# Kernel tuning notes

Measured on AMD Instinct MI355X. Metric: run time of the kernel, lower is better.

## Reference

```python
import jax, jax.numpy as jnp
import numpy as np

ANCHOR_SIZES = (128.0, 256.0, 512.0)
ANCHOR_RATIOS = (0.5, 1.0, 2.0)
IOU_THR = 0.3


def _conv(x, w, b, pad):
    y = jax.lax.conv_general_dilated(
        x, w, window_strides=(1, 1), padding=[(pad, pad), (pad, pad)],
        dimension_numbers=("NCHW", "OIHW", "NCHW"))
    return y + b[None, :, None, None]


def _make_anchors(grid_h, grid_w, stride):
    # torchvision-style cell anchors (ratio-major over scales), rounded
    scales = jnp.asarray(ANCHOR_SIZES, jnp.float32)
    ratios = jnp.asarray(ANCHOR_RATIOS, jnp.float32)
    h_r = jnp.sqrt(ratios)
    w_r = 1.0 / h_r
    ws = (w_r[:, None] * scales[None, :]).reshape(-1)  # (A,)
    hs = (h_r[:, None] * scales[None, :]).reshape(-1)
    base = jnp.round(jnp.stack([-ws, -hs, ws, hs], axis=1) / 2.0)  # (A,4)
    sx = jnp.arange(grid_w, dtype=jnp.float32) * stride
    sy = jnp.arange(grid_h, dtype=jnp.float32) * stride
    yy, xx = jnp.meshgrid(sy, sx, indexing="ij")
    shifts = jnp.stack([xx, yy, xx, yy], axis=-1).reshape(-1, 4)  # (HW,4)
    return (shifts[:, None, :] + base[None, :, :]).reshape(-1, 4)  # (HW*A,4)


def _apply_box(anchors, deltas):
    w = anchors[:, 2] - anchors[:, 0]
    h = anchors[:, 3] - anchors[:, 1]
    cx = anchors[:, 0] + 0.5 * w
    cy = anchors[:, 1] + 0.5 * h
    pcx = deltas[:, 0] * w + cx
    pcy = deltas[:, 1] * h + cy
    pw = jnp.exp(deltas[:, 2]) * w
    ph = jnp.exp(deltas[:, 3]) * h
    return jnp.stack([pcx - 0.5 * pw, pcy - 0.5 * ph,
                      pcx + 0.5 * pw, pcy + 0.5 * ph], axis=1)


def _clip(boxes, img_h, img_w):
    x1 = jnp.clip(boxes[:, 0], 0.0, img_w)
    y1 = jnp.clip(boxes[:, 1], 0.0, img_h)
    x2 = jnp.clip(boxes[:, 2], 0.0, img_w)
    y2 = jnp.clip(boxes[:, 3], 0.0, img_h)
    return jnp.stack([x1, y1, x2, y2], axis=1)


def _nms_keep(boxes, scores, thr):
    # returns boolean keep mask in ORIGINAL box order (all idxs identical in
    # the source's batched_nms call, so this is plain NMS)
    n = boxes.shape[0]
    order = jnp.argsort(-scores)
    b = boxes[order]
    area = (b[:, 2] - b[:, 0]) * (b[:, 3] - b[:, 1])
    lt = jnp.maximum(b[:, None, :2], b[None, :, :2])
    rb = jnp.minimum(b[:, None, 2:], b[None, :, 2:])
    wh = jnp.clip(rb - lt, 0.0, None)
    inter = wh[..., 0] * wh[..., 1]
    iou = inter / (area[:, None] + area[None, :] - inter + 1e-9)  # (N,N)
    idx = jnp.arange(n)

    def body(i, keep):
        sup = (iou[i] > thr) & (idx > i)
        return jnp.where(keep[i], keep & ~sup, keep)

    keep_sorted = jax.lax.fori_loop(0, n, body, jnp.ones(n, bool))
    return jnp.zeros(n, bool).at[order].set(keep_sorted)


def setup_inputs() -> dict:
    key = jax.random.key(0)
    ks = jax.random.split(key, 7)
    C, H, W = 256, 32, 32
    A = len(ANCHOR_SIZES) * len(ANCHOR_RATIOS)  # 9
    return {
        "features": jax.random.normal(ks[0], (1, C, H, W), jnp.float32),
        "image_size": 512,
        "conv_w": jax.random.normal(ks[1], (512, C, 3, 3), jnp.float32) * 0.01,
        "conv_b": jnp.zeros((512,), jnp.float32),
        "cls_w": jax.random.normal(ks[2], (2 * A, 512, 1, 1), jnp.float32) * 0.01,
        "cls_b": jnp.zeros((2 * A,), jnp.float32),
        "bbox_w": jax.random.normal(ks[3], (4 * A, 512, 1, 1), jnp.float32) * 0.01,
        "bbox_b": jnp.zeros((4 * A,), jnp.float32),
    }


def reference(features, image_size, conv_w, conv_b, cls_w, cls_b, bbox_w, bbox_b):
    img_h = img_w = float(image_size)
    x = jax.nn.relu(_conv(features, conv_w, conv_b, pad=1))
    logits = _conv(x, cls_w, cls_b, pad=0)          # (1, 2A, H, W)
    bbox_pred = _conv(x, bbox_w, bbox_b, pad=0)     # (1, 4A, H, W)
    probs = jax.nn.sigmoid(logits)
    fg_scores = probs[:, 1::2, :, :].reshape(-1)    # same flatten order as torch
    grid_h, grid_w = features.shape[2], features.shape[3]
    stride = image_size // grid_h
    anchors = _make_anchors(grid_h, grid_w, float(stride))
    proposals = _apply_box(anchors, bbox_pred.reshape(-1, 4))
    proposals = _clip(proposals, img_h, img_w)
    keep = _nms_keep(proposals, fg_scores, IOU_THR)
    # fixed-shape output: suppressed boxes zeroed, plus the keep mask
    return proposals * keep[:, None].astype(proposals.dtype), probs, keep
```

## Files before the change

kernel.cpp:

```cpp
#include <hip/hip_runtime.h>
#include <math.h>

#define X_B      0
#define BBOX_B   2097152
#define PROPS_B  2244608
#define KEYS_B   2392064
#define RANK_B   2465792
#define SKEYS_B  2502656
#define SBOX_B   2576384
#define MASK_B   2725888
#define WS_NEED  13400000

typedef unsigned long long u64;
typedef double v4d __attribute__((ext_vector_type(4)));

__global__ __launch_bounds__(256, 2) void conv3x3_mfma_k(
    const float* __restrict__ feat, const float* __restrict__ w,
    const float* __restrict__ bias, float* __restrict__ xout)
{
  __shared__ float wl[9280];
  __shared__ float fl[8768];

  const int tid = threadIdx.x;
  const int bid = blockIdx.x;
  const int ct = ((bid & 7) << 2) | ((bid >> 3) >> 4);
  const int g  = (bid >> 3) & 15;
  const int co0 = ct << 4;
  const int y0  = g << 1;

  for (int i = tid; i < 8768; i += 256) fl[i] = 0.0f;

  const int lane = tid & 63, wv = tid >> 6;
  const int q = lane >> 4, n = lane & 15;
  const int wy = wv >> 1, xb = (wv & 1) << 4;
  const int xn = xb + n;

  v4d ac0 = {0.0, 0.0, 0.0, 0.0}, ac1 = {0.0, 0.0, 0.0, 0.0};
  v4d ac2 = {0.0, 0.0, 0.0, 0.0}, ac3 = {0.0, 0.0, 0.0, 0.0};
  const float4* feat4 = (const float4*)feat;

  __syncthreads();

  for (int c = 0; c < 4; ++c) {
    const int cb = c << 6;
    #pragma unroll
    for (int i = 0; i < 9; ++i) {
      const int idx4 = tid + (i << 8);
      const int co = idx4 / 144;
      const int s4 = idx4 - co * 144;
      *(float4*)&wl[co * 580 + (s4 << 2)] =
          *(const float4*)(w + (co0 + co) * 2304 + c * 576 + (s4 << 2));
    }
    #pragma unroll
    for (int i = 0; i < 8; ++i) {
      const int idx4 = tid + (i << 8);
      const int ci = idx4 >> 5;
      const int rr = (idx4 >> 3) & 3;
      const int x4 = idx4 & 7;
      const int grow = y0 - 1 + rr;
      if ((unsigned)grow < 32u) {
        const float4 v = feat4[((cb + ci) << 8) + (grow << 3) + x4];
        float* p = &fl[ci * 137 + rr * 34 + 1 + (x4 << 2)];
        p[0] = v.x; p[1] = v.y; p[2] = v.z; p[3] = v.w;
      }
    }
    __syncthreads();
    #pragma unroll
    for (int tap = 0; tap < 9; ++tap) {
      const int ky = tap / 3, kx = tap - 3 * (tap / 3);
      const float* ab = &wl[n * 580 + q * 9 + tap];
      const float* bb = &fl[q * 137 + (wy + ky) * 34 + xn + kx];
      #pragma unroll
      for (int u = 0; u < 16; u += 4) {
        ac0 = __builtin_amdgcn_mfma_f64_16x16x4f64(
            (double)ab[(u + 0) * 36], (double)bb[(u + 0) * 548], ac0, 0, 0, 0);
        ac1 = __builtin_amdgcn_mfma_f64_16x16x4f64(
            (double)ab[(u + 1) * 36], (double)bb[(u + 1) * 548], ac1, 0, 0, 0);
        ac2 = __builtin_amdgcn_mfma_f64_16x16x4f64(
            (double)ab[(u + 2) * 36], (double)bb[(u + 2) * 548], ac2, 0, 0, 0);
        ac3 = __builtin_amdgcn_mfma_f64_16x16x4f64(
            (double)ab[(u + 3) * 36], (double)bb[(u + 3) * 548], ac3, 0, 0, 0);
      }
    }
    __syncthreads();
  }

  const int pbase = (g << 6) + (wv << 4) + n;
  #pragma unroll
  for (int i = 0; i < 4; ++i) {
    const int co = co0 + q + (i << 2);
    const double s = (ac0[i] + ac1[i]) + (ac2[i] + ac3[i]);
    const double v = fmax(s + (double)bias[co], 0.0);
    xout[(co << 10) + pbase] = (float)v;
  }
}

#define CPITCH 38
#define CCHS   (18 * CPITCH)
__global__ __launch_bounds__(256) void conv3x3_relu_fb_k(
    const float* __restrict__ feat, const float* __restrict__ w,
    const float* __restrict__ bias, float* __restrict__ xout)
{
  __shared__ float il[2][8 * CCHS];
  const int cp = blockIdx.x >> 1, h = blockIdx.x & 1;
  const int tid = threadIdx.x;
  const int h16 = h << 4;
  const int co0 = cp << 1;
  for (int i = tid; i < 8 * CCHS; i += 256) { il[0][i] = 0.0f; il[1][i] = 0.0f; }
  const int yl = tid >> 4;
  const int x0 = (tid & 15) << 1;
  double aA0 = 0.0, aA1 = 0.0, aB0 = 0.0, aB1 = 0.0;
  const float4* feat4 = (const float4*)feat;
  float4 pf[5]; int pch[5], pt[5], pc4[5], pok[5];
  #pragma unroll
  for (int k = 0; k < 5; ++k) {
    const int i = tid + (k << 8);
    const int ch = i / 144, rem = i - ch * 144;
    const int t = rem >> 3, c4 = rem & 7;
    const int g = h16 - 1 + t;
    pch[k] = ch; pt[k] = t; pc4[k] = c4;
    pok[k] = (i < 1152) && ((unsigned)g < 32u);
    pf[k] = pok[k] ? feat4[(ch << 8) + (g << 3) + c4] : float4{0.f,0.f,0.f,0.f};
  }
  __syncthreads();
  for (int cc = 0; cc < 256; cc += 8) {
    const int buf = (cc >> 3) & 1;
    #pragma unroll
    for (int k = 0; k < 5; ++k)
      if (pok[k]) {
        float* p = &il[buf][pch[k] * CCHS + pt[k] * CPITCH + (pc4[k] << 2) + 1];
        p[0] = pf[k].x; p[1] = pf[k].y; p[2] = pf[k].z; p[3] = pf[k].w;
      }
    if (cc + 8 < 256) {
      #pragma unroll
      for (int k = 0; k < 5; ++k) {
        const int g = h16 - 1 + pt[k];
        if (pok[k]) pf[k] = feat4[((cc + 8 + pch[k]) << 8) + (g << 3) + pc4[k]];
      }
    }
    __syncthreads();
    #pragma unroll
    for (int cl = 0; cl < 8; ++cl) {
      const float* wAp = w + co0 * 2304 + (cc + cl) * 9;
      const float* wBp = wAp + 2304;
      double wa[9], wb[9];
      #pragma unroll
      for (int q = 0; q < 9; ++q) { wa[q] = (double)wAp[q]; wb[q] = (double)wBp[q]; }
      const float* ir = &il[buf][cl * CCHS + yl * CPITCH + x0];
      #pragma unroll
      for (int ky = 0; ky < 3; ++ky) {
        const float2 q0 = *(const float2*)(ir + ky * CPITCH);
        const float2 q1 = *(const float2*)(ir + ky * CPITCH + 2);
        const double v0 = (double)q0.x, v1 = (double)q0.y;
        const double v2 = (double)q1.x, v3 = (double)q1.y;
        aA0 += v0 * wa[3*ky+0] + v1 * wa[3*ky+1] + v2 * wa[3*ky+2];
        aA1 += v1 * wa[3*ky+0] + v2 * wa[3*ky+1] + v3 * wa[3*ky+2];
        aB0 += v0 * wb[3*ky+0] + v1 * wb[3*ky+1] + v2 * wb[3*ky+2];
        aB1 += v1 * wb[3*ky+0] + v2 * wb[3*ky+1] + v3 * wb[3*ky+2];
      }
    }
  }
  const double bA = (double)bias[co0], bB = (double)bias[co0 + 1];
  const int y = h16 + yl;
  float2 rA, rB;
  rA.x = (float)fmax(aA0 + bA, 0.0); rA.y = (float)fmax(aA1 + bA, 0.0);
  rB.x = (float)fmax(aB0 + bB, 0.0); rB.y = (float)fmax(aB1 + bB, 0.0);
  *(float2*)&xout[(co0 << 10) + (y << 5) + x0] = rA;
  *(float2*)&xout[((co0 + 1) << 10) + (y << 5) + x0] = rB;
}

__global__ __launch_bounds__(256) void head1x1_k(
    const float* __restrict__ x,
    const float* __restrict__ cls_w, const float* __restrict__ cls_b,
    const float* __restrict__ bbox_w, const float* __restrict__ bbox_b,
    float* __restrict__ out, float* __restrict__ bbox_out)
{
  __shared__ float wl[512];
  const int bid = blockIdx.x;
  const int co = bid >> 2;
  const int px = ((bid & 3) << 8) | threadIdx.x;
  const bool is_cls = co < 18;
  const float* wsrc = is_cls ? (cls_w + co * 512) : (bbox_w + (co - 18) * 512);
  for (int i = threadIdx.x; i < 512; i += 256) wl[i] = wsrc[i];
  __syncthreads();
  double acc0 = 0.0, acc1 = 0.0, acc2 = 0.0, acc3 = 0.0;
  #pragma unroll 4
  for (int c = 0; c < 512; c += 4) {
    acc0 += (double)x[((c + 0) << 10) | px] * (double)wl[c + 0];
    acc1 += (double)x[((c + 1) << 10) | px] * (double)wl[c + 1];
    acc2 += (double)x[((c + 2) << 10) | px] * (double)wl[c + 2];
    acc3 += (double)x[((c + 3) << 10) | px] * (double)wl[c + 3];
  }
  double acc = ((acc0 + acc1) + (acc2 + acc3)) +
               (double)(is_cls ? cls_b[co] : bbox_b[co - 18]);
  if (is_cls)
    out[36864 + (co << 10) + px] = (float)(1.0 / (1.0 + exp(-acc)));
  else
    bbox_out[((co - 18) << 10) + px] = (float)acc;
}

__global__ __launch_bounds__(256) void proposals_k(
    const float* __restrict__ bbox, const int* __restrict__ imgsz,
    const float* __restrict__ out, float* __restrict__ props,
    u64* __restrict__ keys, unsigned* __restrict__ rank)
{
  const int r = blockIdx.x * 256 + threadIdx.x;
  if (r >= 9216) return;
  const float4 d = ((const float4*)bbox)[r];
  const int cell = r / 9, a = r - cell * 9;
  const int ix = cell & 31, iy = cell >> 5;
  const int ri = a / 3, si = a - ri * 3;
  const double ratio = (ri == 0) ? 0.5 : (ri == 1 ? 1.0 : 2.0);
  const double scale = (si == 0) ? 128.0 : (si == 1 ? 256.0 : 512.0);
  const double hr = sqrt(ratio), wr = 1.0 / hr;
  const double bx = nearbyint(wr * scale * 0.5);
  const double by = nearbyint(hr * scale * 0.5);
  const double cx = ix * 16.0, cy = iy * 16.0;
  const double w = 2.0 * bx, hh = 2.0 * by;
  const double pcx = (double)d.x * w + cx;
  const double pcy = (double)d.y * hh + cy;
  const double pw = exp((double)d.z) * w;
  const double ph = exp((double)d.w) * hh;
  const double im = (double)imgsz[0];
  float4 o;
  o.x = (float)fmin(fmax(pcx - 0.5 * pw, 0.0), im);
  o.y = (float)fmin(fmax(pcy - 0.5 * ph, 0.0), im);
  o.z = (float)fmin(fmax(pcx + 0.5 * pw, 0.0), im);
  o.w = (float)fmin(fmax(pcy + 0.5 * ph, 0.0), im);
  ((float4*)props)[r] = o;
  const float s = out[36864 + ((2 * (r >> 10) + 1) << 10) + (r & 1023)];
  keys[r] = ((u64)__float_as_uint(s) << 32) | (unsigned)(0x7FFFFFFF - r);
  rank[r] = 0u;
}

__global__ __launch_bounds__(256) void rank_k(
    const u64* __restrict__ keys, unsigned* __restrict__ rank)
{
  const int jt = blockIdx.x % 36, ic = blockIdx.x / 36;
  const int j = jt * 256 + threadIdx.x;
  const u64 kj = keys[j];
  const int lane = threadIdx.x & 63;
  const int base = ic * 576;
  unsigned lo[9], hi[9];
  #pragma unroll
  for (int rr = 0; rr < 9; ++rr) {
    const u64 k = keys[base + rr * 64 + lane];
    lo[rr] = (unsigned)k; hi[rr] = (unsigned)(k >> 32);
  }
  unsigned cnt = 0;
  #pragma unroll
  for (int rr = 0; rr < 9; ++rr) {
    #pragma unroll
    for (int l = 0; l < 64; ++l) {
      const unsigned llo = (unsigned)__builtin_amdgcn_readlane((int)lo[rr], l);
      const unsigned lhi = (unsigned)__builtin_amdgcn_readlane((int)hi[rr], l);
      const u64 ki = ((u64)lhi << 32) | llo;
      cnt += (ki > kj) ? 1u : 0u;
    }
  }
  atomicAdd(&rank[j], cnt);
}

__global__ __launch_bounds__(256) void scatter_k(
    const u64* __restrict__ keys, const unsigned* __restrict__ rank,
    const float* __restrict__ props, u64* __restrict__ skeys,
    float4* __restrict__ sboxes)
{
  const int r = blockIdx.x * 256 + threadIdx.x;
  if (r >= 9216) return;
  const unsigned rk = rank[r];
  skeys[rk] = keys[r];
  sboxes[rk] = ((const float4*)props)[r];
}

__global__ __launch_bounds__(256) void mask_k(
    const float4* __restrict__ sb4, u64* __restrict__ mask)
{
  __shared__ __align__(16) float4 ib[64];
  const int ci = blockIdx.x;
  const int Wb = blockIdx.y << 2;
  const int i_lo = ci << 6;
  const int i_hi = min(i_lo + 64, (Wb + 4) << 6);
  if (i_lo >= i_hi) return;
  const int wv = threadIdx.x >> 6, lane = threadIdx.x & 63;
  const int W = Wb + wv;
  const int cnt = i_hi - i_lo;
  if (threadIdx.x < cnt) ib[threadIdx.x] = sb4[i_lo + threadIdx.x];
  __syncthreads();
  const float4 bj = sb4[(W << 6) + lane];
  const float areaJ = (bj.z - bj.x) * (bj.w - bj.y);
  const int n = i_hi - i_lo;
  #pragma unroll 8
  for (int k = 0; k < n; ++k) {
    const float4 bi = ib[k];
    const float areaI = (bi.z - bi.x) * (bi.w - bi.y);
    const float ix1 = fmaxf(bj.x, bi.x), iy1 = fmaxf(bj.y, bi.y);
    const float ix2 = fminf(bj.z, bi.z), iy2 = fminf(bj.w, bi.w);
    const float iw = fmaxf(ix2 - ix1, 0.0f), ih = fmaxf(iy2 - iy1, 0.0f);
    const double inter = (double)iw * (double)ih;
    const double uni = (double)areaJ + (double)areaI - inter + 1e-9;
    const bool pred = inter > 0.3 * uni;
    const u64 bal = __ballot(pred);
    const int i = i_lo + k;
    if (lane == 0) mask[(size_t)i * 144 + W] = bal;
  }
}

__global__ __launch_bounds__(1024) void sweep_out_k(
    const u64* __restrict__ mask, const u64* __restrict__ skeys,
    const float4* __restrict__ sboxes, float* __restrict__ out)
{
  extern __shared__ __align__(16) char sm[];
  u64* subm   = (u64*)sm;
  u64* supAll = subm + 9216;
  u64* keptS  = supAll + 144;
  unsigned short* kpl = (unsigned short*)(keptS + 144);
  int* kcnt  = (int*)(kpl + 9216);
  int* kprev = kcnt + 1;

  const int tid = threadIdx.x;
  const int lane = tid & 63, wv = tid >> 6;
  if (tid == 0) { *kcnt = 0; *kprev = 0; }
  if (tid < 144) { keptS[tid] = 0ULL; supAll[tid] = 0ULL; }
  if (tid < 512) {
    const int wq = tid & 7, r0 = tid >> 3;
    #pragma unroll
    for (int k = 0; k < 8; ++k) {
      const int i = r0 + (k << 6);
      subm[i * 9 + wq] = mask[(size_t)i * 144 + wq];
    }
  }
  __syncthreads();

  for (int sg = 0; sg < 18; ++sg) {
    const int buf = sg & 1;
    const int wbase = sg << 3;
    const int ibase = wbase << 6;
    const int P = *kprev, K = *kcnt;
    if (K > P) {
      const int nW = 144 - wbase;
      const int S = 1024 / nW;
      const int wi = tid % nW, sl = tid / nW;
      if (sl < S) {
        u64 acc = 0ULL;
        for (int j = P + sl; j < K; j += S)
          acc |= mask[(size_t)kpl[j] * 144 + wbase + wi];
        if (acc) atomicOr(&supAll[wbase + wi], acc);
      }
    }
    __syncthreads();
    if (wv == 0) {
      u64 myAlive = (lane < 8) ? ~supAll[wbase + lane] : 0ULL;
      const u64* sub = subm + buf * 4608;
      for (int w = 0; w < 8; ++w) {
        const u64 av = __shfl(myAlive, w, 64);
        if (av == 0ULL) continue;
        const u64 rowL = sub[((w << 6) + lane) * 9 + w];
        u64 cand = av, keptw = 0ULL;
        while (cand) {
          const int b = (int)__builtin_ctzll(cand);
          keptw |= 1ULL << b;
          const u64 sup =
              ((u64)(unsigned)__builtin_amdgcn_readlane((int)(rowL >> 32), b)
               << 32) |
              (unsigned)__builtin_amdgcn_readlane((int)rowL, b);
          cand &= ~(sup | (1ULL << b));
        }
        if (lane == 0) keptS[wbase + w] = keptw;
        if (keptw) {
          const int K2 = *kcnt;
          if ((keptw >> lane) & 1ULL) {
            const int pre =
                __builtin_popcountll(keptw & ((1ULL << lane) - 1ULL));
            kpl[K2 + pre] = (unsigned short)(ibase + (w << 6) + lane);
          }
          if (lane == 0) *kcnt = K2 + __builtin_popcountll(keptw);
          u64 t = keptw;
          while (t) {
            int bs[8]; int nn = 0;
            #pragma unroll
            for (int s = 0; s < 8; ++s) {
              if (t) { bs[s] = (int)__builtin_ctzll(t); t &= t - 1ULL; nn = s + 1; }
              else bs[s] = 0;
            }
            const int kk = lane >> 3, wq = lane & 7;
            u64 r = (kk < nn) ? sub[((w << 6) + bs[kk]) * 9 + wq] : 0ULL;
            r |= __shfl_down(r, 8, 64);
            r |= __shfl_down(r, 16, 64);
            r |= __shfl_down(r, 32, 64);
            myAlive &= ~r;
          }
        }
      }
    } else if (wv == 1) {
      if (lane == 0) *kprev = K;
    } else if (wv >= 8 && sg + 1 < 18) {
      const int s = tid - 512;
      const int wq = s & 7, r0 = s >> 3;
      const int nb = 1 - buf;
      const int ib2 = (sg + 1) << 9;
      const int wb2 = (sg + 1) << 3;
      #pragma unroll
      for (int k = 0; k < 8; ++k) {
        const int i = r0 + (k << 6);
        subm[nb * 4608 + i * 9 + wq] = mask[(size_t)(ib2 + i) * 144 + wb2 + wq];
      }
    }
    __syncthreads();
  }
  for (int i = tid; i < 9216; i += 1024) {
    const u64 key = skeys[i];
    const int orig = 0x7FFFFFFF - (int)(unsigned)(key & 0xFFFFFFFFULL);
    const bool kp = (keptS[i >> 6] >> (i & 63)) & 1ULL;
    float4 ob = sboxes[i];
    if (!kp) { ob.x = 0.f; ob.y = 0.f; ob.z = 0.f; ob.w = 0.f; }
    ((float4*)out)[orig] = ob;
    out[55296 + orig] = kp ? 1.0f : 0.0f;
  }
}

__global__ __launch_bounds__(1024) void nms_fallback_k(
    const float* __restrict__ props, float* __restrict__ out)
{
  __shared__ u64 wmax[16];
  __shared__ float4 curBoxS;
  const int tid = threadIdx.x, wid = tid >> 6, lane = tid & 63;
  u64 key[9];
  float4 box[9];
  #pragma unroll
  for (int j = 0; j < 9; ++j) {
    const int r = tid + (j << 10);
    box[j] = ((const float4*)props)[r];
    const float s = out[36864 + ((2 * (r >> 10) + 1) << 10) + (r & 1023)];
    key[j] = ((u64)__float_as_uint(s) << 32) | (unsigned)(0x7FFFFFFF - r);
  }
  unsigned kept = 0;
  for (;;) {
    u64 m = key[0];
    #pragma unroll
    for (int j = 1; j < 9; ++j) m = key[j] > m ? key[j] : m;
    #pragma unroll
    for (int off = 32; off; off >>= 1) {
      const u64 o = __shfl_down(m, off, 64);
      if (o > m) m = o;
    }
    if (lane == 0) wmax[wid] = m;
    __syncthreads();
    u64 K = wmax[0];
    #pragma unroll
    for (int wv2 = 1; wv2 < 16; ++wv2) { const u64 t = wmax[wv2]; if (t > K) K = t; }
    if (K == 0) break;
    #pragma unroll
    for (int j = 0; j < 9; ++j)
      if (key[j] == K) { curBoxS = box[j]; key[j] = 0; kept |= 1u << j; }
    __syncthreads();
    const float4 cb = curBoxS;
    const float areaC = (cb.z - cb.x) * (cb.w - cb.y);
    #pragma unroll
    for (int j = 0; j < 9; ++j) {
      if (key[j]) {
        const float4 b = box[j];
        const float ix1 = fmaxf(b.x, cb.x), iy1 = fmaxf(b.y, cb.y);
        const float ix2 = fminf(b.z, cb.z), iy2 = fminf(b.w, cb.w);
        const float iw = fmaxf(ix2 - ix1, 0.0f), ih = fmaxf(iy2 - iy1, 0.0f);
        const float areaB = (b.z - b.x) * (b.w - b.y);
        const double inter = (double)iw * (double)ih;
        const double uni = (double)areaB + (double)areaC - inter + 1e-9;
        if (inter > 0.3 * uni) key[j] = 0;
      }
    }
    __syncthreads();
  }
  #pragma unroll
  for (int j = 0; j < 9; ++j) {
    const int r = tid + (j << 10);
    const bool kp = (kept >> j) & 1u;
    float4 ob = box[j];
    if (!kp) { ob.x = 0.f; ob.y = 0.f; ob.z = 0.f; ob.w = 0.f; }
    ((float4*)out)[r] = ob;
    out[55296 + r] = kp ? 1.0f : 0.0f;
  }
}

extern "C" void kernel_launch(void* const* d_in, const int* in_sizes, int n_in,
                              void* d_out, int out_size, void* d_ws, size_t ws_size,
                              hipStream_t stream)
{
  const float* feat   = (const float*)d_in[0];
  const int*   imgsz  = (const int*)d_in[1];
  const float* conv_w = (const float*)d_in[2];
  const float* conv_b = (const float*)d_in[3];
  const float* cls_w  = (const float*)d_in[4];
  const float* cls_b  = (const float*)d_in[5];
  const float* bbox_w = (const float*)d_in[6];
  const float* bbox_b = (const float*)d_in[7];
  float* out = (float*)d_out;
  char*  ws  = (char*)d_ws;
  float* x      = (float*)(ws + X_B);
  float* bbox   = (float*)(ws + BBOX_B);
  float* props  = (float*)(ws + PROPS_B);
  u64*      keys  = (u64*)(ws + KEYS_B);
  unsigned* rankp = (unsigned*)(ws + RANK_B);
  u64*      skeys = (u64*)(ws + SKEYS_B);
  float4*   sboxs = (float4*)(ws + SBOX_B);
  u64*      maskp = (u64*)(ws + MASK_B);

  if (ws_size >= (size_t)WS_NEED) {
    hipLaunchKernelGGL(conv3x3_mfma_k, dim3(512), dim3(256), 0, stream,
                       feat, conv_w, conv_b, x);
    hipLaunchKernelGGL(head1x1_k, dim3(216), dim3(256), 0, stream,
                       x, cls_w, cls_b, bbox_w, bbox_b, out, bbox);
    hipLaunchKernelGGL(proposals_k, dim3(36), dim3(256), 0, stream,
                       bbox, imgsz, out, props, keys, rankp);
    hipLaunchKernelGGL(rank_k, dim3(576), dim3(256), 0, stream, keys, rankp);
    hipLaunchKernelGGL(scatter_k, dim3(36), dim3(256), 0, stream,
                       keys, rankp, props, skeys, sboxs);
    hipLaunchKernelGGL(mask_k, dim3(144, 36), dim3(256), 0, stream,
                       sboxs, maskp);
    hipLaunchKernelGGL(sweep_out_k, dim3(1), dim3(1024), 94472, stream,
                       maskp, skeys, sboxs, out);
  } else {
    hipLaunchKernelGGL(conv3x3_relu_fb_k, dim3(512), dim3(256), 0, stream,
                       feat, conv_w, conv_b, x);
    hipLaunchKernelGGL(head1x1_k, dim3(216), dim3(256), 0, stream,
                       x, cls_w, cls_b, bbox_w, bbox_b, out, bbox);
    hipLaunchKernelGGL(proposals_k, dim3(36), dim3(256), 0, stream,
                       bbox, imgsz, out, props, keys, rankp);
    hipLaunchKernelGGL(nms_fallback_k, dim3(1), dim3(1024), 0, stream,
                       props, out);
  }
}
```

Measured before the change: 257.4 us.

## Pipeline suppression accumulation for next segment alongside serial NMS sweep

The single-block NMS sweep now keeps only a double-buffered 8-word suppression vector instead of the full 144-word array. It accumulates the next segment's suppression from already-kept boxes in idle waves 2-7 while wave 0 runs the serial greedy sweep, so the per-segment gather then only covers boxes newly kept in the current segment. It also preloads the diagonal rows into registers and unrolls the word loop. In exchange the code is more complex, with split 32-bit atomics and buffer-clearing logic that must be ordered correctly.

```diff
diff --git a/kernel.cpp b/kernel.cpp
--- a/kernel.cpp
+++ b/kernel.cpp
@@ -312,8 +312,8 @@
 {
   extern __shared__ __align__(16) char sm[];
   u64* subm   = (u64*)sm;
-  u64* supAll = subm + 9216;
-  u64* keptS  = supAll + 144;
+  u64* supS   = subm + 9216;
+  u64* keptS  = supS + 16;
   unsigned short* kpl = (unsigned short*)(keptS + 144);
   int* kcnt  = (int*)(kpl + 9216);
   int* kprev = kcnt + 1;
@@ -321,7 +321,8 @@
   const int tid = threadIdx.x;
   const int lane = tid & 63, wv = tid >> 6;
   if (tid == 0) { *kcnt = 0; *kprev = 0; }
-  if (tid < 144) { keptS[tid] = 0ULL; supAll[tid] = 0ULL; }
+  if (tid < 144) keptS[tid] = 0ULL;
+  if (tid < 16) supS[tid] = 0ULL;
   if (tid < 512) {
     const int wq = tid & 7, r0 = tid >> 3;
     #pragma unroll
@@ -333,29 +334,34 @@
   __syncthreads();
 
   for (int sg = 0; sg < 18; ++sg) {
-    const int buf = sg & 1;
+    const int buf = sg & 1, nb = buf ^ 1;
     const int wbase = sg << 3;
     const int ibase = wbase << 6;
     const int P = *kprev, K = *kcnt;
     if (K > P) {
-      const int nW = 144 - wbase;
-      const int S = 1024 / nW;
-      const int wi = tid % nW, sl = tid / nW;
-      if (sl < S) {
-        u64 acc = 0ULL;
-        for (int j = P + sl; j < K; j += S)
-          acc |= mask[(size_t)kpl[j] * 144 + wbase + wi];
-        if (acc) atomicOr(&supAll[wbase + wi], acc);
-      }
-    }
+      const int wq = tid & 7, str = tid >> 3;
+      u64 acc = 0ULL;
+      for (int j = P + str; j < K; j += 128)
+        acc |= mask[(size_t)kpl[j] * 144 + wbase + wq];
+      if (acc) {
+        atomicOr((unsigned*)&supS[(buf << 3) + wq], (unsigned)acc);
+        atomicOr(((unsigned*)&supS[(buf << 3) + wq]) + 1, (unsigned)(acc >> 32));
+      }
+    }
+    if (tid >= 1008) ((unsigned*)&supS[nb << 3])[tid - 1008] = 0u;
     __syncthreads();
     if (wv == 0) {
-      u64 myAlive = (lane < 8) ? ~supAll[wbase + lane] : 0ULL;
+      u64 myAlive = (lane < 8) ? ~supS[(buf << 3) + lane] : 0ULL;
       const u64* sub = subm + buf * 4608;
+      u64 rowL8[8];
+      #pragma unroll
+      for (int w = 0; w < 8; ++w)
+        rowL8[w] = sub[((w << 6) + lane) * 9 + w];
+      #pragma unroll
       for (int w = 0; w < 8; ++w) {
         const u64 av = __shfl(myAlive, w, 64);
         if (av == 0ULL) continue;
-        const u64 rowL = sub[((w << 6) + lane) * 9 + w];
+        const u64 rowL = rowL8[w];
         u64 cand = av, keptw = 0ULL;
         while (cand) {
           const int b = (int)__builtin_ctzll(cand);
@@ -394,10 +400,30 @@
       }
     } else if (wv == 1) {
       if (lane == 0) *kprev = K;
-    } else if (wv >= 8 && sg + 1 < 18) {
+    } else if (wv < 8) {
+      if (sg + 1 < 18 && K > 0) {
+        const int t6 = tid - 128;
+        const int wq = t6 & 7, str = t6 >> 3;
+        const int wb2 = (sg + 1) << 3;
+        u64 acc = 0ULL;
+        int j = str;
+        for (; j + 3 * 48 < K; j += 4 * 48) {
+          const u64 a0 = mask[(size_t)kpl[j + 0 * 48] * 144 + wb2 + wq];
+          const u64 a1 = mask[(size_t)kpl[j + 1 * 48] * 144 + wb2 + wq];
+          const u64 a2 = mask[(size_t)kpl[j + 2 * 48] * 144 + wb2 + wq];
+          const u64 a3 = mask[(size_t)kpl[j + 3 * 48] * 144 + wb2 + wq];
+          acc |= (a0 | a1) | (a2 | a3);
+        }
+        for (; j < K; j += 48)
+          acc |= mask[(size_t)kpl[j] * 144 + wb2 + wq];
+        if (acc) {
+          atomicOr((unsigned*)&supS[(nb << 3) + wq], (unsigned)acc);
+          atomicOr(((unsigned*)&supS[(nb << 3) + wq]) + 1, (unsigned)(acc >> 32));
+        }
+      }
+    } else if (sg + 1 < 18) {
       const int s = tid - 512;
       const int wq = s & 7, r0 = s >> 3;
-      const int nb = 1 - buf;
       const int ib2 = (sg + 1) << 9;
       const int wb2 = (sg + 1) << 3;
       #pragma unroll
@@ -517,7 +543,7 @@
                        keys, rankp, props, skeys, sboxs);
     hipLaunchKernelGGL(mask_k, dim3(144, 36), dim3(256), 0, stream,
                        sboxs, maskp);
-    hipLaunchKernelGGL(sweep_out_k, dim3(1), dim3(1024), 94472, stream,
+    hipLaunchKernelGGL(sweep_out_k, dim3(1), dim3(1024), 93448, stream,
                        maskp, skeys, sboxs, out);
   } else {
     hipLaunchKernelGGL(conv3x3_relu_fb_k, dim3(512), dim3(256), 0, stream,
```

After: 251.3 us. -2.3%, faster.
